# Optimization experiments

Measured on AMD Instinct MI355X. Metric: run time of the kernel, lower is better.

The kernel has to match this reference:

```python
import jax, jax.numpy as jnp
import numpy as np

N = 50000
E = 800000
IN_C = 128
HID = 16
HEADS = 8
OUT_C = 64
NEG_SLOPE = 0.2


def setup_inputs() -> dict:
    key = jax.random.key(0)
    ks = jax.random.split(key, 12)
    x = jax.random.normal(ks[0], (N, IN_C), dtype=jnp.float32)
    edge_index = jax.random.randint(ks[1], (2, E), 0, N, dtype=jnp.int32)
    s = 0.1
    W1 = jax.random.normal(ks[2], (IN_C, HEADS * HID), dtype=jnp.float32) * s
    a1_src = jax.random.normal(ks[3], (HEADS, HID), dtype=jnp.float32) * s
    a1_dst = jax.random.normal(ks[4], (HEADS, HID), dtype=jnp.float32) * s
    b1 = jnp.zeros((HEADS * HID,), dtype=jnp.float32)
    W2 = jax.random.normal(ks[5], (HEADS * HID, OUT_C), dtype=jnp.float32) * s
    a2_src = jax.random.normal(ks[6], (1, OUT_C), dtype=jnp.float32) * s
    a2_dst = jax.random.normal(ks[7], (1, OUT_C), dtype=jnp.float32) * s
    b2 = jnp.zeros((OUT_C,), dtype=jnp.float32)
    return {"x": x, "edge_index": edge_index, "W1": W1, "a1_src": a1_src,
            "a1_dst": a1_dst, "b1": b1, "W2": W2, "a2_src": a2_src,
            "a2_dst": a2_dst, "b2": b2}


def gat_conv(x, src, dst, W, a_src, a_dst, b, heads, ch):
    # linear projection -> [N, H, C]
    h = (x @ W).reshape(N, heads, ch)
    # per-node attention logits [N, H]
    al_s = jnp.einsum('nhc,hc->nh', h, a_src)
    al_d = jnp.einsum('nhc,hc->nh', h, a_dst)
    # per-edge logits [E, H]
    e = jax.nn.leaky_relu(al_s[src] + al_d[dst], NEG_SLOPE)
    # segment softmax over incoming edges of each dst node
    emax = jax.ops.segment_max(e, dst, num_segments=N)
    ee = jnp.exp(e - emax[dst])
    denom = jax.ops.segment_sum(ee, dst, num_segments=N)
    alpha = ee / (denom[dst] + 1e-16)
    # weighted scatter-aggregate of source messages
    msg = h[src] * alpha[:, :, None]  # [E, H, C]
    out = jax.ops.segment_sum(msg, dst, num_segments=N)
    return out.reshape(N, heads * ch) + b


def reference(x, edge_index, W1, a1_src, a1_dst, b1, W2, a2_src, a2_dst, b2):
    # add self loops (PyG GATConv default add_self_loops=True)
    loops = jnp.arange(N, dtype=edge_index.dtype)
    src = jnp.concatenate([edge_index[0], loops])
    dst = jnp.concatenate([edge_index[1], loops])
    h = gat_conv(x, src, dst, W1, a1_src, a1_dst, b1, HEADS, HID)
    h = jax.nn.relu(h)
    # dropout p=0.6 is identity in eval mode
    out = gat_conv(h, src, dst, W2, a2_src, a2_dst, b2, 1, OUT_C)
    return out
```

## Files before the change

### kernel.cpp

```cpp
#include <hip/hip_runtime.h>
#include <hip/hip_fp16.h>
#include <math.h>

#define N_NODES 50000
#define E_EDGES 800000
#define IN_C    128
#define HID     16
#define HEADS   8
#define OUT_C   64
#define NEG_SLOPE 0.2f
#define NSHARD  8
#define SHW     24
#define CELLW   64

typedef _Float16 half8 __attribute__((ext_vector_type(8)));
typedef float floatx4 __attribute__((ext_vector_type(4)));

#define XCC_ID_REG (((4 - 1) << 11) | 20)

__device__ __forceinline__ float lrelu_exp(float v) {
    v = v > 0.f ? v : NEG_SLOPE * v;
    return __expf(v);
}

__global__ __launch_bounds__(256) void fused_gemm_fill(
    const float* __restrict__ X, const float* __restrict__ W, __half* __restrict__ H,
    const float* __restrict__ a_src, const float* __restrict__ a_dst,
    float* __restrict__ als, float* __restrict__ ald,
    const int* __restrict__ src, const int* __restrict__ dst,
    int* __restrict__ cursor, int* __restrict__ ell) {
    __shared__ _Float16 wT[IN_C * 136];
    const int bid = blockIdx.x;
    const int t = threadIdx.x;

    if (bid & 1) {
        const int xcc = __builtin_amdgcn_s_getreg(XCC_ID_REG) & 7;
        int* cur = cursor + xcc * N_NODES;
        int* es = ell + (size_t)xcc * N_NODES * SHW;
        const int tid = (bid >> 1) * 256 + t;
        if (tid < E_EDGES / 4) {
            const int4 s4 = ((const int4*)src)[tid];
            const int4 d4 = ((const int4*)dst)[tid];
            const int p0 = atomicAdd(&cur[d4.x], 1);
            const int p1 = atomicAdd(&cur[d4.y], 1);
            const int p2 = atomicAdd(&cur[d4.z], 1);
            const int p3 = atomicAdd(&cur[d4.w], 1);
            if (p0 < SHW) es[d4.x * SHW + p0] = s4.x;
            if (p1 < SHW) es[d4.y * SHW + p1] = s4.y;
            if (p2 < SHW) es[d4.z * SHW + p2] = s4.z;
            if (p3 < SHW) es[d4.w * SHW + p3] = s4.w;
        }
        return;
    }

    for (int f = t * 4; f < IN_C * IN_C; f += 1024) {
        const float4 w4 = *(const float4*)&W[f];
        const int k = f >> 7, col = f & 127;
        wT[(col + 0) * 136 + k] = (_Float16)w4.x;
        wT[(col + 1) * 136 + k] = (_Float16)w4.y;
        wT[(col + 2) * 136 + k] = (_Float16)w4.z;
        wT[(col + 3) * 136 + k] = (_Float16)w4.w;
    }
    __syncthreads();

    const int wave = t >> 6, lane = t & 63;
    const int m = lane & 15, quad = lane >> 4;
    const int r0w = (bid >> 1) * 64 + wave * 16;
    int rl = r0w + m;
    if (rl >= N_NODES) rl = N_NODES - 1;
    const float* Xr = X + (size_t)rl * IN_C;

    floatx4 acc[8];
#pragma unroll
    for (int i = 0; i < 8; ++i) acc[i] = (floatx4){0.f, 0.f, 0.f, 0.f};

#pragma unroll
    for (int kc = 0; kc < 4; ++kc) {
        const int k8 = kc * 32 + quad * 8;
        const float4 xa = *(const float4*)(Xr + k8);
        const float4 xb = *(const float4*)(Xr + k8 + 4);
        half8 a;
        a[0] = (_Float16)xa.x; a[1] = (_Float16)xa.y;
        a[2] = (_Float16)xa.z; a[3] = (_Float16)xa.w;
        a[4] = (_Float16)xb.x; a[5] = (_Float16)xb.y;
        a[6] = (_Float16)xb.z; a[7] = (_Float16)xb.w;
#pragma unroll
        for (int ct = 0; ct < 8; ++ct) {
            const half8 b = *(const half8*)&wT[(ct * 16 + m) * 136 + k8];
            acc[ct] = __builtin_amdgcn_mfma_f32_16x16x32_f16(a, b, acc[ct], 0, 0, 0);
        }
    }

    _Float16* Hh = (_Float16*)H;
#pragma unroll
    for (int ct = 0; ct < 8; ++ct) {
        const float asv = a_src[ct * 16 + m];
        const float adv = a_dst[ct * 16 + m];
#pragma unroll
        for (int r = 0; r < 4; ++r) {
            const int row = r0w + quad * 4 + r;
            const float c = acc[ct][r];
            float ps = c * asv, pd = c * adv;
            ps += __shfl_xor(ps, 1); pd += __shfl_xor(pd, 1);
            ps += __shfl_xor(ps, 2); pd += __shfl_xor(pd, 2);
            ps += __shfl_xor(ps, 4); pd += __shfl_xor(pd, 4);
            ps += __shfl_xor(ps, 8); pd += __shfl_xor(pd, 8);
            if (row < N_NODES) {
                Hh[(size_t)row * IN_C + ct * 16 + m] = (_Float16)c;
                if (m == 0) {
                    als[(size_t)row * HEADS + ct] = ps;
                    ald[(size_t)row * HEADS + ct] = pd;
                }
            }
        }
    }
}

__global__ __launch_bounds__(256) void compact_ell(
    const int* __restrict__ cursor, const int* __restrict__ ell_sh,
    int* __restrict__ cnt_tot, int* __restrict__ ell_c) {
    const int gt = blockIdx.x * 256 + threadIdx.x;
    const int n = gt >> 3, sh = gt & 7;
    if (n >= N_NODES) return;
    int c = cursor[sh * N_NODES + n];
    c = c < SHW ? c : SHW;
    int pre = c;
#pragma unroll
    for (int off = 1; off < 8; off <<= 1) {
        int v = __shfl_up(pre, off, 8);
        if ((threadIdx.x & 7) >= off) pre += v;
    }
    const int base = pre - c;
    if (sh == 7) cnt_tot[n] = pre;
    const int* inp = ell_sh + ((size_t)sh * N_NODES + n) * SHW;
    int* outp = ell_c + (size_t)n * CELLW + base;
    for (int j = 0; j < c; j += 4) {
        const int4 v = *(const int4*)(inp + j);
        outp[j] = v.x;
        if (j + 1 < c) outp[j + 1] = v.y;
        if (j + 2 < c) outp[j + 2] = v.z;
        if (j + 3 < c) outp[j + 3] = v.w;
    }
}

__global__ __launch_bounds__(256) void agg1_gemm2(
    const int* __restrict__ cnt, const int* __restrict__ ell,
    const float* __restrict__ als, const float* __restrict__ ald,
    const __half* __restrict__ H, const float* __restrict__ b,
    const float* __restrict__ W2, const float* __restrict__ a2_src,
    const float* __restrict__ a2_dst, __half* __restrict__ H2,
    float* __restrict__ als2, float* __restrict__ ald2) {
    __shared__ _Float16 wsh[IN_C * OUT_C];
    __shared__ float xrow[32 * 132];
    const int t = threadIdx.x;
    for (int f = t * 4; f < IN_C * OUT_C; f += 1024) {
        const float4 w4 = *(const float4*)&W2[f];
        wsh[f + 0] = (_Float16)w4.x;
        wsh[f + 1] = (_Float16)w4.y;
        wsh[f + 2] = (_Float16)w4.z;
        wsh[f + 3] = (_Float16)w4.w;
    }

    const int nl = t >> 3, h = t & 7;
    int nc = blockIdx.x * 32 + nl;
    if (nc >= N_NODES) nc = N_NODES - 1;
    const int deg = cnt[nc];
    const int* ep = ell + (size_t)nc * CELLW;
    const float ad = ald[nc * HEADS + h];
    float accv[16];
    float ssum;
    {
        const float w = lrelu_exp(als[nc * HEADS + h] + ad);
        const half8* q = (const half8*)(H + ((size_t)nc * HEADS + h) * HID);
        const half8 u0 = q[0], u1 = q[1];
        ssum = w;
#pragma unroll
        for (int j = 0; j < 8; ++j) {
            accv[j] = w * (float)u0[j];
            accv[j + 8] = w * (float)u1[j];
        }
    }
    for (int p = 0; p < deg; p += 4) {
        const int4 s4 = *(const int4*)(ep + p);
        const int i1 = (p + 1 < deg) ? s4.y : nc;
        const int i2 = (p + 2 < deg) ? s4.z : nc;
        const int i3 = (p + 3 < deg) ? s4.w : nc;
        const float f1 = (p + 1 < deg) ? 1.f : 0.f;
        const float f2 = (p + 2 < deg) ? 1.f : 0.f;
        const float f3 = (p + 3 < deg) ? 1.f : 0.f;
        const float v0 = als[s4.x * HEADS + h];
        const float v1 = als[i1 * HEADS + h];
        const float v2 = als[i2 * HEADS + h];
        const float v3 = als[i3 * HEADS + h];
        const half8* q0 = (const half8*)(H + ((size_t)s4.x * HEADS + h) * HID);
        const half8* q1 = (const half8*)(H + ((size_t)i1 * HEADS + h) * HID);
        const half8* q2 = (const half8*)(H + ((size_t)i2 * HEADS + h) * HID);
        const half8* q3 = (const half8*)(H + ((size_t)i3 * HEADS + h) * HID);
        const half8 a0 = q0[0], b0 = q0[1];
        const half8 a1 = q1[0], b1 = q1[1];
        const half8 a2 = q2[0], b2 = q2[1];
        const half8 a3 = q3[0], b3 = q3[1];
        const float w0 = lrelu_exp(v0 + ad);
        const float w1 = lrelu_exp(v1 + ad) * f1;
        const float w2 = lrelu_exp(v2 + ad) * f2;
        const float w3 = lrelu_exp(v3 + ad) * f3;
        ssum += (w0 + w1) + (w2 + w3);
#pragma unroll
        for (int j = 0; j < 8; ++j) {
            accv[j]     += w0 * (float)a0[j] + w1 * (float)a1[j] +
                           w2 * (float)a2[j] + w3 * (float)a3[j];
            accv[j + 8] += w0 * (float)b0[j] + w1 * (float)b1[j] +
                           w2 * (float)b2[j] + w3 * (float)b3[j];
        }
    }
    {
        const float inv = 1.f / (ssum + 1e-16f);
        float* xr = &xrow[nl * 132 + h * 16];
#pragma unroll
        for (int j = 0; j < 16; ++j) {
            float r = accv[j] * inv + b[h * 16 + j];
            xr[j] = r > 0.f ? r : 0.f;
        }
    }

    __syncthreads();

    const int ng = t >> 3, jc = t & 7, j0 = jc * 8;
    const int n2 = blockIdx.x * 32 + ng;
    float o[8] = {};
    const float* xb = &xrow[ng * 132];
#pragma unroll 2
    for (int c = 0; c < IN_C; ++c) {
        const float xv = xb[c];
        const half8 wv = *(const half8*)&wsh[c * OUT_C + j0];
#pragma unroll
        for (int k = 0; k < 8; ++k) o[k] += xv * (float)wv[k];
    }
    float ps = 0.f, pd = 0.f;
#pragma unroll
    for (int k = 0; k < 8; ++k) {
        ps += o[k] * a2_src[j0 + k];
        pd += o[k] * a2_dst[j0 + k];
    }
    ps += __shfl_xor(ps, 1); pd += __shfl_xor(pd, 1);
    ps += __shfl_xor(ps, 2); pd += __shfl_xor(pd, 2);
    ps += __shfl_xor(ps, 4); pd += __shfl_xor(pd, 4);
    if (n2 < N_NODES) {
        half8 hv;
#pragma unroll
        for (int k = 0; k < 8; ++k) hv[k] = (_Float16)o[k];
        *(half8*)((_Float16*)H2 + (size_t)n2 * OUT_C + j0) = hv;
        if (jc == 0) {
            als2[n2] = ps;
            ald2[n2] = pd;
        }
    }
}

__global__ __launch_bounds__(256) void agg2(
    const int* __restrict__ cnt, const int* __restrict__ ell,
    const float* __restrict__ als, const float* __restrict__ ald,
    const __half* __restrict__ H, const float* __restrict__ b,
    float* __restrict__ out) {
    const int t = threadIdx.x;
    int n = blockIdx.x * 32 + (t >> 3);
    const int j0 = (t & 7) * 8;
    const bool valid = n < N_NODES;
    if (!valid) n = N_NODES - 1;
    const int deg = cnt[n];
    const int* ep = ell + (size_t)n * CELLW;
    const float ad = ald[n];
    float accv[8];
    float ssum;
    {
        const float w = lrelu_exp(als[n] + ad);
        const half8 u = *(const half8*)(H + (size_t)n * OUT_C + j0);
        ssum = w;
#pragma unroll
        for (int k = 0; k < 8; ++k) accv[k] = w * (float)u[k];
    }
    for (int p = 0; p < deg; p += 4) {
        const int4 s4 = *(const int4*)(ep + p);
        const int i1 = (p + 1 < deg) ? s4.y : n;
        const int i2 = (p + 2 < deg) ? s4.z : n;
        const int i3 = (p + 3 < deg) ? s4.w : n;
        const float f1 = (p + 1 < deg) ? 1.f : 0.f;
        const float f2 = (p + 2 < deg) ? 1.f : 0.f;
        const float f3 = (p + 3 < deg) ? 1.f : 0.f;
        const float v0 = als[s4.x];
        const float v1 = als[i1];
        const float v2 = als[i2];
        const float v3 = als[i3];
        const half8 u0 = *(const half8*)(H + (size_t)s4.x * OUT_C + j0);
        const half8 u1 = *(const half8*)(H + (size_t)i1 * OUT_C + j0);
        const half8 u2 = *(const half8*)(H + (size_t)i2 * OUT_C + j0);
        const half8 u3 = *(const half8*)(H + (size_t)i3 * OUT_C + j0);
        const float w0 = lrelu_exp(v0 + ad);
        const float w1 = lrelu_exp(v1 + ad) * f1;
        const float w2 = lrelu_exp(v2 + ad) * f2;
        const float w3 = lrelu_exp(v3 + ad) * f3;
        ssum += (w0 + w1) + (w2 + w3);
#pragma unroll
        for (int k = 0; k < 8; ++k)
            accv[k] += w0 * (float)u0[k] + w1 * (float)u1[k] +
                       w2 * (float)u2[k] + w3 * (float)u3[k];
    }
    if (valid) {
        const float inv = 1.f / (ssum + 1e-16f);
        float4 r0, r1;
        r0.x = accv[0] * inv + b[j0 + 0]; r0.y = accv[1] * inv + b[j0 + 1];
        r0.z = accv[2] * inv + b[j0 + 2]; r0.w = accv[3] * inv + b[j0 + 3];
        r1.x = accv[4] * inv + b[j0 + 4]; r1.y = accv[5] * inv + b[j0 + 5];
        r1.z = accv[6] * inv + b[j0 + 6]; r1.w = accv[7] * inv + b[j0 + 7];
        float* op = out + (size_t)n * OUT_C + j0;
        *(float4*)op = r0;
        *(float4*)(op + 4) = r1;
    }
}

extern "C" void kernel_launch(void* const* d_in, const int* in_sizes, int n_in,
                              void* d_out, int out_size, void* d_ws, size_t ws_size,
                              hipStream_t stream) {
    const float* x      = (const float*)d_in[0];
    const int*   ei     = (const int*)d_in[1];
    const float* W1     = (const float*)d_in[2];
    const float* a1_src = (const float*)d_in[3];
    const float* a1_dst = (const float*)d_in[4];
    const float* b1     = (const float*)d_in[5];
    const float* W2     = (const float*)d_in[6];
    const float* a2_src = (const float*)d_in[7];
    const float* a2_dst = (const float*)d_in[8];
    const float* b2     = (const float*)d_in[9];
    const int* src = ei;
    const int* dst = ei + E_EDGES;
    float* outp = (float*)d_out;

    char* wsb = (char*)d_ws;
    __half* h1   = (__half*)wsb;
    __half* h2   = h1 + (size_t)N_NODES * IN_C;
    float*  als1 = (float*)(h2 + (size_t)N_NODES * OUT_C);
    float*  ald1 = als1 + N_NODES * HEADS;
    float*  als2 = ald1 + N_NODES * HEADS;
    float*  ald2 = als2 + N_NODES;
    int*    cursor  = (int*)(ald2 + N_NODES);
    int*    ell_sh  = cursor + NSHARD * N_NODES;
    int*    cnt_tot = ell_sh + (size_t)NSHARD * N_NODES * SHW;
    int*    ell_c   = cnt_tot + N_NODES;

    hipMemsetAsync(cursor, 0, NSHARD * N_NODES * sizeof(int), stream);

    {
        const int gemm_blocks = (N_NODES + 63) / 64;
        fused_gemm_fill<<<gemm_blocks * 2, 256, 0, stream>>>(
            x, W1, h1, a1_src, a1_dst, als1, ald1, src, dst, cursor, ell_sh);
    }

    compact_ell<<<(N_NODES * 8 + 255) / 256, 256, 0, stream>>>(cursor, ell_sh,
                                                               cnt_tot, ell_c);

    agg1_gemm2<<<(N_NODES + 31) / 32, 256, 0, stream>>>(
        cnt_tot, ell_c, als1, ald1, h1, b1, W2, a2_src, a2_dst, h2, als2, ald2);

    agg2<<<(N_NODES + 31) / 32, 256, 0, stream>>>(cnt_tot, ell_c, als2, ald2, h2, b2, outp);
}
```

Measured before the change: 223.2 us.

## Pack per-shard edge buckets into 64-byte rows with 16-bit source indices

```diff
diff --git a/kernel.cpp b/kernel.cpp
--- a/kernel.cpp
+++ b/kernel.cpp
@@ -10,10 +10,12 @@
 #define OUT_C   64
 #define NEG_SLOPE 0.2f
 #define NSHARD  8
-#define SHW     24
+#define ROWB    64
+#define SHSLOT  30
 #define CELLW   64
 
 typedef _Float16 half8 __attribute__((ext_vector_type(8)));
+typedef _Float16 half4 __attribute__((ext_vector_type(4)));
 typedef float floatx4 __attribute__((ext_vector_type(4)));
 
 #define XCC_ID_REG (((4 - 1) << 11) | 20)
@@ -28,38 +30,46 @@
     const float* __restrict__ a_src, const float* __restrict__ a_dst,
     float* __restrict__ als, float* __restrict__ ald,
     const int* __restrict__ src, const int* __restrict__ dst,
-    int* __restrict__ cursor, int* __restrict__ ell) {
+    unsigned* __restrict__ ell_sh) {
     __shared__ _Float16 wT[IN_C * 136];
     const int bid = blockIdx.x;
     const int t = threadIdx.x;
 
     if (bid & 1) {
         const int xcc = __builtin_amdgcn_s_getreg(XCC_ID_REG) & 7;
-        int* cur = cursor + xcc * N_NODES;
-        int* es = ell + (size_t)xcc * N_NODES * SHW;
+        char* base = (char*)ell_sh + (size_t)xcc * N_NODES * ROWB;
         const int tid = (bid >> 1) * 256 + t;
         if (tid < E_EDGES / 4) {
             const int4 s4 = ((const int4*)src)[tid];
             const int4 d4 = ((const int4*)dst)[tid];
-            const int p0 = atomicAdd(&cur[d4.x], 1);
-            const int p1 = atomicAdd(&cur[d4.y], 1);
-            const int p2 = atomicAdd(&cur[d4.z], 1);
-            const int p3 = atomicAdd(&cur[d4.w], 1);
-            if (p0 < SHW) es[d4.x * SHW + p0] = s4.x;
-            if (p1 < SHW) es[d4.y * SHW + p1] = s4.y;
-            if (p2 < SHW) es[d4.z * SHW + p2] = s4.z;
-            if (p3 < SHW) es[d4.w * SHW + p3] = s4.w;
+            unsigned* r0 = (unsigned*)(base + (size_t)d4.x * ROWB);
+            unsigned* r1 = (unsigned*)(base + (size_t)d4.y * ROWB);
+            unsigned* r2 = (unsigned*)(base + (size_t)d4.z * ROWB);
+            unsigned* r3 = (unsigned*)(base + (size_t)d4.w * ROWB);
+            const unsigned p0 = atomicAdd(r0, 1u);
+            const unsigned p1 = atomicAdd(r1, 1u);
+            const unsigned p2 = atomicAdd(r2, 1u);
+            const unsigned p3 = atomicAdd(r3, 1u);
+            if (p0 < SHSLOT) ((unsigned short*)(r0 + 1))[p0] = (unsigned short)s4.x;
+            if (p1 < SHSLOT) ((unsigned short*)(r1 + 1))[p1] = (unsigned short)s4.y;
+            if (p2 < SHSLOT) ((unsigned short*)(r2 + 1))[p2] = (unsigned short)s4.z;
+            if (p3 < SHSLOT) ((unsigned short*)(r3 + 1))[p3] = (unsigned short)s4.w;
         }
         return;
     }
 
-    for (int f = t * 4; f < IN_C * IN_C; f += 1024) {
-        const float4 w4 = *(const float4*)&W[f];
-        const int k = f >> 7, col = f & 127;
-        wT[(col + 0) * 136 + k] = (_Float16)w4.x;
-        wT[(col + 1) * 136 + k] = (_Float16)w4.y;
-        wT[(col + 2) * 136 + k] = (_Float16)w4.z;
-        wT[(col + 3) * 136 + k] = (_Float16)w4.w;
+    {
+        const int col = t & 127;
+        const int kq = (t >> 7) * 4;
+        for (int it = 0; it < 16; ++it) {
+            const int k0 = it * 8 + kq;
+            half4 hv;
+            hv[0] = (_Float16)W[(size_t)(k0 + 0) * IN_C + col];
+            hv[1] = (_Float16)W[(size_t)(k0 + 1) * IN_C + col];
+            hv[2] = (_Float16)W[(size_t)(k0 + 2) * IN_C + col];
+            hv[3] = (_Float16)W[(size_t)(k0 + 3) * IN_C + col];
+            *(half4*)&wT[col * 136 + k0] = hv;
+        }
     }
     __syncthreads();
 
@@ -117,34 +127,32 @@
 }
 
 __global__ __launch_bounds__(256) void compact_ell(
-    const int* __restrict__ cursor, const int* __restrict__ ell_sh,
-    int* __restrict__ cnt_tot, int* __restrict__ ell_c) {
+    const unsigned* __restrict__ ell_sh, int* __restrict__ cnt_tot,
+    unsigned short* __restrict__ ell_c) {
     const int gt = blockIdx.x * 256 + threadIdx.x;
     const int n = gt >> 3, sh = gt & 7;
     if (n >= N_NODES) return;
-    int c = cursor[sh * N_NODES + n];
-    c = c < SHW ? c : SHW;
+    const unsigned* row = (const unsigned*)((const char*)ell_sh +
+                                            ((size_t)sh * N_NODES + n) * ROWB);
+    int c = (int)row[0];
+    c = c < SHSLOT ? c : SHSLOT;
     int pre = c;
 #pragma unroll
     for (int off = 1; off < 8; off <<= 1) {
         int v = __shfl_up(pre, off, 8);
         if ((threadIdx.x & 7) >= off) pre += v;
     }
-    const int base = pre - c;
-    if (sh == 7) cnt_tot[n] = pre;
-    const int* inp = ell_sh + ((size_t)sh * N_NODES + n) * SHW;
-    int* outp = ell_c + (size_t)n * CELLW + base;
-    for (int j = 0; j < c; j += 4) {
-        const int4 v = *(const int4*)(inp + j);
-        outp[j] = v.x;
-        if (j + 1 < c) outp[j + 1] = v.y;
-        if (j + 2 < c) outp[j + 2] = v.z;
-        if (j + 3 < c) outp[j + 3] = v.w;
-    }
+    int base = pre - c;
+    if (sh == 7) cnt_tot[n] = pre < CELLW ? pre : CELLW;
+    if (base > CELLW) base = CELLW;
+    int cw = c < (CELLW - base) ? c : (CELLW - base);
+    const unsigned short* slots = (const unsigned short*)(row + 1);
+    unsigned short* outp = ell_c + (size_t)n * CELLW + base;
+    for (int j = 0; j < cw; ++j) outp[j] = slots[j];
 }
 
 __global__ __launch_bounds__(256) void agg1_gemm2(
-    const int* __restrict__ cnt, const int* __restrict__ ell,
+    const int* __restrict__ cnt, const unsigned short* __restrict__ ell,
     const float* __restrict__ als, const float* __restrict__ ald,
     const __half* __restrict__ H, const float* __restrict__ b,
     const float* __restrict__ W2, const float* __restrict__ a2_src,
@@ -165,7 +173,7 @@
     int nc = blockIdx.x * 32 + nl;
     if (nc >= N_NODES) nc = N_NODES - 1;
     const int deg = cnt[nc];
-    const int* ep = ell + (size_t)nc * CELLW;
+    const unsigned short* ep = ell + (size_t)nc * CELLW;
     const float ad = ald[nc * HEADS + h];
     float accv[16];
     float ssum;
@@ -181,18 +189,22 @@
         }
     }
     for (int p = 0; p < deg; p += 4) {
-        const int4 s4 = *(const int4*)(ep + p);
-        const int i1 = (p + 1 < deg) ? s4.y : nc;
-        const int i2 = (p + 2 < deg) ? s4.z : nc;
-        const int i3 = (p + 3 < deg) ? s4.w : nc;
+        const int2 qv = *(const int2*)(ep + p);
+        const int s0 = qv.x & 0xffff;
+        const int s1u = (qv.x >> 16) & 0xffff;
+        const int s2u = qv.y & 0xffff;
+        const int s3u = (qv.y >> 16) & 0xffff;
+        const int i1 = (p + 1 < deg) ? s1u : nc;
+        const int i2 = (p + 2 < deg) ? s2u : nc;
+        const int i3 = (p + 3 < deg) ? s3u : nc;
         const float f1 = (p + 1 < deg) ? 1.f : 0.f;
         const float f2 = (p + 2 < deg) ? 1.f : 0.f;
         const float f3 = (p + 3 < deg) ? 1.f : 0.f;
-        const float v0 = als[s4.x * HEADS + h];
+        const float v0 = als[s0 * HEADS + h];
         const float v1 = als[i1 * HEADS + h];
         const float v2 = als[i2 * HEADS + h];
         const float v3 = als[i3 * HEADS + h];
-        const half8* q0 = (const half8*)(H + ((size_t)s4.x * HEADS + h) * HID);
+        const half8* q0 = (const half8*)(H + ((size_t)s0 * HEADS + h) * HID);
         const half8* q1 = (const half8*)(H + ((size_t)i1 * HEADS + h) * HID);
         const half8* q2 = (const half8*)(H + ((size_t)i2 * HEADS + h) * HID);
         const half8* q3 = (const half8*)(H + ((size_t)i3 * HEADS + h) * HID);
@@ -258,7 +270,7 @@
 }
 
 __global__ __launch_bounds__(256) void agg2(
-    const int* __restrict__ cnt, const int* __restrict__ ell,
+    const int* __restrict__ cnt, const unsigned short* __restrict__ ell,
     const float* __restrict__ als, const float* __restrict__ ald,
     const __half* __restrict__ H, const float* __restrict__ b,
     float* __restrict__ out) {
@@ -268,7 +280,7 @@
     const bool valid = n < N_NODES;
     if (!valid) n = N_NODES - 1;
     const int deg = cnt[n];
-    const int* ep = ell + (size_t)n * CELLW;
+    const unsigned short* ep = ell + (size_t)n * CELLW;
     const float ad = ald[n];
     float accv[8];
     float ssum;
@@ -280,18 +292,22 @@
         for (int k = 0; k < 8; ++k) accv[k] = w * (float)u[k];
     }
     for (int p = 0; p < deg; p += 4) {
-        const int4 s4 = *(const int4*)(ep + p);
-        const int i1 = (p + 1 < deg) ? s4.y : n;
-        const int i2 = (p + 2 < deg) ? s4.z : n;
-        const int i3 = (p + 3 < deg) ? s4.w : n;
+        const int2 qv = *(const int2*)(ep + p);
+        const int s0 = qv.x & 0xffff;
+        const int s1u = (qv.x >> 16) & 0xffff;
+        const int s2u = qv.y & 0xffff;
+        const int s3u = (qv.y >> 16) & 0xffff;
+        const int i1 = (p + 1 < deg) ? s1u : n;
+        const int i2 = (p + 2 < deg) ? s2u : n;
+        const int i3 = (p + 3 < deg) ? s3u : n;
         const float f1 = (p + 1 < deg) ? 1.f : 0.f;
         const float f2 = (p + 2 < deg) ? 1.f : 0.f;
         const float f3 = (p + 3 < deg) ? 1.f : 0.f;
-        const float v0 = als[s4.x];
+        const float v0 = als[s0];
         const float v1 = als[i1];
         const float v2 = als[i2];
         const float v3 = als[i3];
-        const half8 u0 = *(const half8*)(H + (size_t)s4.x * OUT_C + j0);
+        const half8 u0 = *(const half8*)(H + (size_t)s0 * OUT_C + j0);
         const half8 u1 = *(const half8*)(H + (size_t)i1 * OUT_C + j0);
         const half8 u2 = *(const half8*)(H + (size_t)i2 * OUT_C + j0);
         const half8 u3 = *(const half8*)(H + (size_t)i3 * OUT_C + j0);
@@ -342,21 +358,19 @@
     float*  ald1 = als1 + N_NODES * HEADS;
     float*  als2 = ald1 + N_NODES * HEADS;
     float*  ald2 = als2 + N_NODES;
-    int*    cursor  = (int*)(ald2 + N_NODES);
-    int*    ell_sh  = cursor + NSHARD * N_NODES;
-    int*    cnt_tot = ell_sh + (size_t)NSHARD * N_NODES * SHW;
-    int*    ell_c   = cnt_tot + N_NODES;
-
-    hipMemsetAsync(cursor, 0, NSHARD * N_NODES * sizeof(int), stream);
+    int*    cnt_tot = (int*)(ald2 + N_NODES);
+    unsigned short* ell_c = (unsigned short*)(cnt_tot + N_NODES);
+    unsigned* ell_sh = (unsigned*)(ell_c + (size_t)N_NODES * CELLW);
+
+    hipMemsetAsync(ell_sh, 0, (size_t)NSHARD * N_NODES * ROWB, stream);
 
     {
         const int gemm_blocks = (N_NODES + 63) / 64;
         fused_gemm_fill<<<gemm_blocks * 2, 256, 0, stream>>>(
-            x, W1, h1, a1_src, a1_dst, als1, ald1, src, dst, cursor, ell_sh);
-    }
-
-    compact_ell<<<(N_NODES * 8 + 255) / 256, 256, 0, stream>>>(cursor, ell_sh,
-                                                               cnt_tot, ell_c);
+            x, W1, h1, a1_src, a1_dst, als1, ald1, src, dst, ell_sh);
+    }
+
+    compact_ell<<<(N_NODES * 8 + 255) / 256, 256, 0, stream>>>(ell_sh, cnt_tot, ell_c);
 
     agg1_gemm2<<<(N_NODES + 31) / 32, 256, 0, stream>>>(
         cnt_tot, ell_c, als1, ald1, h1, b1, W2, a2_src, a2_dst, h2, als2, ald2);
```

Measured after the change: 275.0 us. 23.2% more time.

## Replace per-XCC sharded ELL build with single global ELL and drop compaction kernel

Applied to the files above, without the earlier changes.

```diff
diff --git a/kernel.cpp b/kernel.cpp
--- a/kernel.cpp
+++ b/kernel.cpp
@@ -9,14 +9,11 @@
 #define HEADS   8
 #define OUT_C   64
 #define NEG_SLOPE 0.2f
-#define NSHARD  8
-#define SHW     24
 #define CELLW   64
 
 typedef _Float16 half8 __attribute__((ext_vector_type(8)));
+typedef _Float16 half4 __attribute__((ext_vector_type(4)));
 typedef float floatx4 __attribute__((ext_vector_type(4)));
-
-#define XCC_ID_REG (((4 - 1) << 11) | 20)
 
 __device__ __forceinline__ float lrelu_exp(float v) {
     v = v > 0.f ? v : NEG_SLOPE * v;
@@ -34,32 +31,34 @@
     const int t = threadIdx.x;
 
     if (bid & 1) {
-        const int xcc = __builtin_amdgcn_s_getreg(XCC_ID_REG) & 7;
-        int* cur = cursor + xcc * N_NODES;
-        int* es = ell + (size_t)xcc * N_NODES * SHW;
         const int tid = (bid >> 1) * 256 + t;
         if (tid < E_EDGES / 4) {
             const int4 s4 = ((const int4*)src)[tid];
             const int4 d4 = ((const int4*)dst)[tid];
-            const int p0 = atomicAdd(&cur[d4.x], 1);
-            const int p1 = atomicAdd(&cur[d4.y], 1);
-            const int p2 = atomicAdd(&cur[d4.z], 1);
-            const int p3 = atomicAdd(&cur[d4.w], 1);
-            if (p0 < SHW) es[d4.x * SHW + p0] = s4.x;
-            if (p1 < SHW) es[d4.y * SHW + p1] = s4.y;
-            if (p2 < SHW) es[d4.z * SHW + p2] = s4.z;
-            if (p3 < SHW) es[d4.w * SHW + p3] = s4.w;
+            const int p0 = atomicAdd(&cursor[d4.x], 1);
+            const int p1 = atomicAdd(&cursor[d4.y], 1);
+            const int p2 = atomicAdd(&cursor[d4.z], 1);
+            const int p3 = atomicAdd(&cursor[d4.w], 1);
+            if (p0 < CELLW) ell[(size_t)d4.x * CELLW + p0] = s4.x;
+            if (p1 < CELLW) ell[(size_t)d4.y * CELLW + p1] = s4.y;
+            if (p2 < CELLW) ell[(size_t)d4.z * CELLW + p2] = s4.z;
+            if (p3 < CELLW) ell[(size_t)d4.w * CELLW + p3] = s4.w;
         }
         return;
     }
 
-    for (int f = t * 4; f < IN_C * IN_C; f += 1024) {
-        const float4 w4 = *(const float4*)&W[f];
-        const int k = f >> 7, col = f & 127;
-        wT[(col + 0) * 136 + k] = (_Float16)w4.x;
-        wT[(col + 1) * 136 + k] = (_Float16)w4.y;
-        wT[(col + 2) * 136 + k] = (_Float16)w4.z;
-        wT[(col + 3) * 136 + k] = (_Float16)w4.w;
+    {
+        const int col = t & 127;
+        const int kq = (t >> 7) * 4;
+        for (int it = 0; it < 16; ++it) {
+            const int k0 = it * 8 + kq;
+            half4 hv;
+            hv[0] = (_Float16)W[(size_t)(k0 + 0) * IN_C + col];
+            hv[1] = (_Float16)W[(size_t)(k0 + 1) * IN_C + col];
+            hv[2] = (_Float16)W[(size_t)(k0 + 2) * IN_C + col];
+            hv[3] = (_Float16)W[(size_t)(k0 + 3) * IN_C + col];
+            *(half4*)&wT[col * 136 + k0] = hv;
+        }
     }
     __syncthreads();
 
@@ -113,33 +112,6 @@
                 }
             }
         }
-    }
-}
-
-__global__ __launch_bounds__(256) void compact_ell(
-    const int* __restrict__ cursor, const int* __restrict__ ell_sh,
-    int* __restrict__ cnt_tot, int* __restrict__ ell_c) {
-    const int gt = blockIdx.x * 256 + threadIdx.x;
-    const int n = gt >> 3, sh = gt & 7;
-    if (n >= N_NODES) return;
-    int c = cursor[sh * N_NODES + n];
-    c = c < SHW ? c : SHW;
-    int pre = c;
-#pragma unroll
-    for (int off = 1; off < 8; off <<= 1) {
-        int v = __shfl_up(pre, off, 8);
-        if ((threadIdx.x & 7) >= off) pre += v;
-    }
-    const int base = pre - c;
-    if (sh == 7) cnt_tot[n] = pre;
-    const int* inp = ell_sh + ((size_t)sh * N_NODES + n) * SHW;
-    int* outp = ell_c + (size_t)n * CELLW + base;
-    for (int j = 0; j < c; j += 4) {
-        const int4 v = *(const int4*)(inp + j);
-        outp[j] = v.x;
-        if (j + 1 < c) outp[j + 1] = v.y;
-        if (j + 2 < c) outp[j + 2] = v.z;
-        if (j + 3 < c) outp[j + 3] = v.w;
     }
 }
 
@@ -164,7 +136,8 @@
     const int nl = t >> 3, h = t & 7;
     int nc = blockIdx.x * 32 + nl;
     if (nc >= N_NODES) nc = N_NODES - 1;
-    const int deg = cnt[nc];
+    int deg = cnt[nc];
+    deg = deg < CELLW ? deg : CELLW;
     const int* ep = ell + (size_t)nc * CELLW;
     const float ad = ald[nc * HEADS + h];
     float accv[16];
@@ -182,17 +155,18 @@
     }
     for (int p = 0; p < deg; p += 4) {
         const int4 s4 = *(const int4*)(ep + p);
+        const int s0 = s4.x;
         const int i1 = (p + 1 < deg) ? s4.y : nc;
         const int i2 = (p + 2 < deg) ? s4.z : nc;
         const int i3 = (p + 3 < deg) ? s4.w : nc;
         const float f1 = (p + 1 < deg) ? 1.f : 0.f;
         const float f2 = (p + 2 < deg) ? 1.f : 0.f;
         const float f3 = (p + 3 < deg) ? 1.f : 0.f;
-        const float v0 = als[s4.x * HEADS + h];
+        const float v0 = als[s0 * HEADS + h];
         const float v1 = als[i1 * HEADS + h];
         const float v2 = als[i2 * HEADS + h];
         const float v3 = als[i3 * HEADS + h];
-        const half8* q0 = (const half8*)(H + ((size_t)s4.x * HEADS + h) * HID);
+        const half8* q0 = (const half8*)(H + ((size_t)s0 * HEADS + h) * HID);
         const half8* q1 = (const half8*)(H + ((size_t)i1 * HEADS + h) * HID);
         const half8* q2 = (const half8*)(H + ((size_t)i2 * HEADS + h) * HID);
         const half8* q3 = (const half8*)(H + ((size_t)i3 * HEADS + h) * HID);
@@ -267,7 +241,8 @@
     const int j0 = (t & 7) * 8;
     const bool valid = n < N_NODES;
     if (!valid) n = N_NODES - 1;
-    const int deg = cnt[n];
+    int deg = cnt[n];
+    deg = deg < CELLW ? deg : CELLW;
     const int* ep = ell + (size_t)n * CELLW;
     const float ad = ald[n];
     float accv[8];
@@ -281,17 +256,18 @@
     }
     for (int p = 0; p < deg; p += 4) {
         const int4 s4 = *(const int4*)(ep + p);
+        const int s0 = s4.x;
         const int i1 = (p + 1 < deg) ? s4.y : n;
         const int i2 = (p + 2 < deg) ? s4.z : n;
         const int i3 = (p + 3 < deg) ? s4.w : n;
         const float f1 = (p + 1 < deg) ? 1.f : 0.f;
         const float f2 = (p + 2 < deg) ? 1.f : 0.f;
         const float f3 = (p + 3 < deg) ? 1.f : 0.f;
-        const float v0 = als[s4.x];
+        const float v0 = als[s0];
         const float v1 = als[i1];
         const float v2 = als[i2];
         const float v3 = als[i3];
-        const half8 u0 = *(const half8*)(H + (size_t)s4.x * OUT_C + j0);
+        const half8 u0 = *(const half8*)(H + (size_t)s0 * OUT_C + j0);
         const half8 u1 = *(const half8*)(H + (size_t)i1 * OUT_C + j0);
         const half8 u2 = *(const half8*)(H + (size_t)i2 * OUT_C + j0);
         const half8 u3 = *(const half8*)(H + (size_t)i3 * OUT_C + j0);
@@ -342,24 +318,20 @@
     float*  ald1 = als1 + N_NODES * HEADS;
     float*  als2 = ald1 + N_NODES * HEADS;
     float*  ald2 = als2 + N_NODES;
-    int*    cursor  = (int*)(ald2 + N_NODES);
-    int*    ell_sh  = cursor + NSHARD * N_NODES;
-    int*    cnt_tot = ell_sh + (size_t)NSHARD * N_NODES * SHW;
-    int*    ell_c   = cnt_tot + N_NODES;
-
-    hipMemsetAsync(cursor, 0, NSHARD * N_NODES * sizeof(int), stream);
+    int*    cursor = (int*)(ald2 + N_NODES);
+    int*    ell    = cursor + N_NODES;
+
+    hipMemsetAsync(cursor, 0, N_NODES * sizeof(int), stream);
 
     {
         const int gemm_blocks = (N_NODES + 63) / 64;
         fused_gemm_fill<<<gemm_blocks * 2, 256, 0, stream>>>(
-            x, W1, h1, a1_src, a1_dst, als1, ald1, src, dst, cursor, ell_sh);
-    }
-
-    compact_ell<<<(N_NODES * 8 + 255) / 256, 256, 0, stream>>>(cursor, ell_sh,
-                                                               cnt_tot, ell_c);
+            x, W1, h1, a1_src, a1_dst, als1, ald1, src, dst, cursor, ell);
+    }
 
     agg1_gemm2<<<(N_NODES + 31) / 32, 256, 0, stream>>>(
-        cnt_tot, ell_c, als1, ald1, h1, b1, W2, a2_src, a2_dst, h2, als2, ald2);
-
-    agg2<<<(N_NODES + 31) / 32, 256, 0, stream>>>(cnt_tot, ell_c, als2, ald2, h2, b2, outp);
-}
+        cursor, ell, als1, ald1, h1, b1, W2, a2_src, a2_dst, h2, als2, ald2);
+
+    agg2<<<(N_NODES + 31) / 32, 256, 0, stream>>>(
+        cursor, ell, als2, ald2, h2, b2, outp);
+}
```

Result: faster. 205.0 us (-8.1%).
